# Performance work log

Hardware: AMD Instinct MI355X
Metric: run time of the kernel (lower is better)

## Reference

```python
import jax, jax.numpy as jnp
import numpy as np

TWO_PI = 2.0 * np.pi

def diff_round(x):
    # smooth differentiable rounding used throughout the repo
    return x - jnp.sin(TWO_PI * x) / TWO_PI

def harder_diff_round(x):
    return diff_round(diff_round(diff_round(x)))

def differentiable_eq(a, b):
    a = harder_diff_round(a)
    b = harder_diff_round(b)
    return harder_diff_round(a * b + (1.0 - a) * (1.0 - b))

def differentiable_and(a, b):
    return diff_round(a) * diff_round(b)

def filter_mask_of_interest(mask, initial_mask_id):
    # mask: [B, N, dx, dy, 4]; initial_mask_id: [B, N, 4]
    c = differentiable_eq(mask, initial_mask_id[:, :, None, None, :])  # [B,N,dx,dy,4]
    a = differentiable_and(c[..., 0], c[..., 1])
    b = differentiable_and(c[..., 2], c[..., 3])
    return differentiable_and(a, b)  # [B, N, dx, dy]

def get_out_image(mask_combined, initial_mask_id, resized_image):
    m = filter_mask_of_interest(mask_combined, initial_mask_id)[..., None]  # [B,N,dx,dy,1]
    masked = m * resized_image
    # per-area masked mean over (dx, dy, channel)
    num = jnp.sum(masked, axis=(2, 3, 4))           # [B, N]
    den = jnp.sum(m, axis=(2, 3, 4))                # [B, N]
    mean = num / den
    return m * mean[:, :, None, None, None]

def setup_inputs() -> dict:
    key = jax.random.key(0)
    k1, k2, k3, k4, k5 = jax.random.split(key, 5)
    B, N, DX, DY = 2, 8192, 16, 16
    return {
        "resized_image": jax.random.uniform(k1, (B, N, DX, DY, 1), jnp.float32),
        "mask_combined": jax.random.uniform(k2, (B, N, DX, DY, 4), jnp.float32),
        "mask_combined_alt": jax.random.uniform(k3, (B, N, DX, DY, 4), jnp.float32),
        "initial_mask_id": jax.random.uniform(k4, (B, N, 4), jnp.float32),
        "mask_new_bi_channel": jax.random.uniform(k5, (B, N, DX, DY, 2), jnp.float32),
        "mask_index": 0,
    }

def reference(resized_image, mask_combined, mask_combined_alt, initial_mask_id, mask_new_bi_channel, mask_index):
    # batched_v_Apply_on_single_area: nested vmap over (batch, area), vectorized here
    out_image = get_out_image(mask_combined, initial_mask_id, resized_image)
    out_image_alt = get_out_image(mask_combined_alt, initial_mask_id, resized_image)
    return (out_image, out_image_alt)
```

## Files before the change

kernel.cpp:

```cpp
#include <hip/hip_runtime.h>

#define INV_2PI 0.15915494309189535f

__device__ __forceinline__ float vsin_pinned(float x) {
    float r;
    asm volatile("v_sin_f32 %0, %1" : "=v"(r) : "v"(x));
    return r;
}

template <int N>
__device__ __forceinline__ void dround_batch(float* c) {
    float s[N];
#pragma unroll
    for (int i = 0; i < N; ++i) s[i] = vsin_pinned(c[i]);
#pragma unroll
    for (int i = 0; i < N; ++i) c[i] = __builtin_fmaf(-INV_2PI, s[i], c[i]);
}

__global__ __launch_bounds__(256) void De_conv_areas_kernel(
    const float* __restrict__ img,
    const float* __restrict__ mask,
    const float* __restrict__ mask_alt,
    const float* __restrict__ mask_id,
    float* __restrict__ out,
    float* __restrict__ out_alt,
    int n_areas)
{
    const int lane = threadIdx.x & 63;
    const int w    = blockIdx.x * (blockDim.x >> 6) + (threadIdx.x >> 6);
    const int area  = w >> 1;
    const int which = w & 1;
    if (area >= n_areas) return;

    const float* msk = which ? mask_alt : mask;
    float*       dst = which ? out_alt  : out;

    const size_t pix = (size_t)area * 256 + (size_t)lane * 4;

    float4 idv = *(const float4*)(mask_id + (size_t)area * 4);
    const float4* mp = (const float4*)(msk + pix * 4);
    float4 p0 = mp[0], p1 = mp[1], p2 = mp[2], p3 = mp[3];
    float4 im = *(const float4*)(img + pix);

    float hb[4] = { idv.x, idv.y, idv.z, idv.w };
    dround_batch<4>(hb); dround_batch<4>(hb); dround_batch<4>(hb);
    float vb[4];
#pragma unroll
    for (int k = 0; k < 4; ++k) vb[k] = 1.0f - hb[k];

    float c[16] = { p0.x, p0.y, p0.z, p0.w,  p1.x, p1.y, p1.z, p1.w,
                    p2.x, p2.y, p2.z, p2.w,  p3.x, p3.y, p3.z, p3.w };

    dround_batch<16>(c); dround_batch<16>(c); dround_batch<16>(c);

#pragma unroll
    for (int i = 0; i < 16; ++i) {
        float om = 1.0f - c[i];
        c[i] = __builtin_fmaf(c[i], hb[i & 3], om * vb[i & 3]);
    }

    dround_batch<16>(c); dround_batch<16>(c); dround_batch<16>(c);

    dround_batch<16>(c);
    float p[8];
#pragma unroll
    for (int j = 0; j < 4; ++j) {
        p[2*j]   = c[4*j]   * c[4*j+1];
        p[2*j+1] = c[4*j+2] * c[4*j+3];
    }
    dround_batch<8>(p);

    float imv[4] = { im.x, im.y, im.z, im.w };
    float m[4];
    float sm = 0.f, si = 0.f;
#pragma unroll
    for (int j = 0; j < 4; ++j) {
        m[j] = p[2*j] * p[2*j+1];
        sm += m[j]; si += m[j] * imv[j];
    }

#pragma unroll
    for (int off = 32; off; off >>= 1) {
        sm += __shfl_xor(sm, off, 64);
        si += __shfl_xor(si, off, 64);
    }

    const float mean = (sm > 0.f) ? (si / sm) : 0.f;

    float4 o;
    o.x = m[0] * mean; o.y = m[1] * mean; o.z = m[2] * mean; o.w = m[3] * mean;
    *(float4*)(dst + pix) = o;
}

extern "C" void kernel_launch(void* const* d_in, const int* in_sizes, int n_in,
                              void* d_out, int out_size, void* d_ws, size_t ws_size,
                              hipStream_t stream) {
    const float* img      = (const float*)d_in[0];
    const float* mask     = (const float*)d_in[1];
    const float* mask_alt = (const float*)d_in[2];
    const float* mask_id  = (const float*)d_in[3];

    const int n_areas = out_size / 512;
    float* out     = (float*)d_out;
    float* out_alt = out + (size_t)n_areas * 256;

    const int n_waves = n_areas * 2;
    const int waves_per_block = 4;
    const int blocks = (n_waves + waves_per_block - 1) / waves_per_block;
    De_conv_areas_kernel<<<blocks, 256, 0, stream>>>(
        img, mask, mask_alt, mask_id, out, out_alt, n_areas);
}
```

Measured before the change: 191.0 us.

## Process both mask variants per wave and share id rounding and image loads

Each wave now handles one area for both the primary and alternate masks instead of one mask per wave. The triple-rounded mask id and the image pixels are therefore computed and loaded once and reused for both outputs. The id rounding is folded into the first 20-wide sine batch, and loads and stores switch to a lane-strided pattern (float4 for masks, scalar for image and output). This halves the wave count and removes the duplicated id and image work. In exchange each thread holds more registers, which may lower occupancy, and the image reads and output writes are now scalar per lane.

```diff
diff --git a/kernel.cpp b/kernel.cpp
--- a/kernel.cpp
+++ b/kernel.cpp
@@ -17,6 +17,26 @@
     for (int i = 0; i < N; ++i) c[i] = __builtin_fmaf(-INV_2PI, s[i], c[i]);
 }
 
+__device__ __forceinline__ void filter_tail(float* c, const float* hb,
+                                            const float* vb, float* m) {
+#pragma unroll
+    for (int i = 0; i < 16; ++i) {
+        float om = 1.0f - c[i];
+        c[i] = __builtin_fmaf(c[i], hb[i & 3], om * vb[i & 3]);
+    }
+    dround_batch<16>(c); dround_batch<16>(c); dround_batch<16>(c);
+    dround_batch<16>(c);
+    float p[8];
+#pragma unroll
+    for (int j = 0; j < 4; ++j) {
+        p[2 * j]     = c[4 * j]     * c[4 * j + 1];
+        p[2 * j + 1] = c[4 * j + 2] * c[4 * j + 3];
+    }
+    dround_batch<8>(p);
+#pragma unroll
+    for (int j = 0; j < 4; ++j) m[j] = p[2 * j] * p[2 * j + 1];
+}
+
 __global__ __launch_bounds__(256) void De_conv_areas_kernel(
     const float* __restrict__ img,
     const float* __restrict__ mask,
@@ -27,69 +47,65 @@
     int n_areas)
 {
     const int lane = threadIdx.x & 63;
-    const int w    = blockIdx.x * (blockDim.x >> 6) + (threadIdx.x >> 6);
-    const int area  = w >> 1;
-    const int which = w & 1;
+    int area = blockIdx.x * (blockDim.x >> 6) + (threadIdx.x >> 6);
     if (area >= n_areas) return;
+    area = __builtin_amdgcn_readfirstlane(area);
 
-    const float* msk = which ? mask_alt : mask;
-    float*       dst = which ? out_alt  : out;
+    const size_t base = (size_t)area * 256;
 
-    const size_t pix = (size_t)area * 256 + (size_t)lane * 4;
+    const float4* mp = (const float4*)mask     + base + lane;
+    const float4* ap = (const float4*)mask_alt + base + lane;
+    const float*  ip = img + base + lane;
 
+    float4 q0 = mp[0], q1 = mp[64], q2 = mp[128], q3 = mp[192];
+    float4 a0 = ap[0], a1 = ap[64], a2 = ap[128], a3 = ap[192];
+    float  i0 = ip[0], i1 = ip[64], i2 = ip[128], i3 = ip[192];
     float4 idv = *(const float4*)(mask_id + (size_t)area * 4);
-    const float4* mp = (const float4*)(msk + pix * 4);
-    float4 p0 = mp[0], p1 = mp[1], p2 = mp[2], p3 = mp[3];
-    float4 im = *(const float4*)(img + pix);
 
-    float hb[4] = { idv.x, idv.y, idv.z, idv.w };
-    dround_batch<4>(hb); dround_batch<4>(hb); dround_batch<4>(hb);
+    float c0[20] = { idv.x, idv.y, idv.z, idv.w,
+                     q0.x, q0.y, q0.z, q0.w,  q1.x, q1.y, q1.z, q1.w,
+                     q2.x, q2.y, q2.z, q2.w,  q3.x, q3.y, q3.z, q3.w };
+    dround_batch<20>(c0); dround_batch<20>(c0); dround_batch<20>(c0);
+
+    float hb[4] = { c0[0], c0[1], c0[2], c0[3] };
     float vb[4];
 #pragma unroll
     for (int k = 0; k < 4; ++k) vb[k] = 1.0f - hb[k];
 
-    float c[16] = { p0.x, p0.y, p0.z, p0.w,  p1.x, p1.y, p1.z, p1.w,
-                    p2.x, p2.y, p2.z, p2.w,  p3.x, p3.y, p3.z, p3.w };
+    float m0[4];
+    filter_tail(c0 + 4, hb, vb, m0);
 
-    dround_batch<16>(c); dround_batch<16>(c); dround_batch<16>(c);
+    float c1[16] = { a0.x, a0.y, a0.z, a0.w,  a1.x, a1.y, a1.z, a1.w,
+                     a2.x, a2.y, a2.z, a2.w,  a3.x, a3.y, a3.z, a3.w };
+    dround_batch<16>(c1); dround_batch<16>(c1); dround_batch<16>(c1);
+    float m1[4];
+    filter_tail(c1, hb, vb, m1);
 
+    float im[4] = { i0, i1, i2, i3 };
+    float sm0 = 0.f, si0 = 0.f, sm1 = 0.f, si1 = 0.f;
 #pragma unroll
-    for (int i = 0; i < 16; ++i) {
-        float om = 1.0f - c[i];
-        c[i] = __builtin_fmaf(c[i], hb[i & 3], om * vb[i & 3]);
+    for (int j = 0; j < 4; ++j) {
+        sm0 += m0[j]; si0 += m0[j] * im[j];
+        sm1 += m1[j]; si1 += m1[j] * im[j];
+    }
+#pragma unroll
+    for (int off = 32; off; off >>= 1) {
+        sm0 += __shfl_xor(sm0, off, 64);
+        si0 += __shfl_xor(si0, off, 64);
+        sm1 += __shfl_xor(sm1, off, 64);
+        si1 += __shfl_xor(si1, off, 64);
     }
 
-    dround_batch<16>(c); dround_batch<16>(c); dround_batch<16>(c);
+    const float mean0 = (sm0 > 0.f) ? (si0 / sm0) : 0.f;
+    const float mean1 = (sm1 > 0.f) ? (si1 / sm1) : 0.f;
 
-    dround_batch<16>(c);
-    float p[8];
+    float* d0 = out     + base + lane;
+    float* d1 = out_alt + base + lane;
 #pragma unroll
-    for (int j = 0; j < 4; ++j) {
-        p[2*j]   = c[4*j]   * c[4*j+1];
-        p[2*j+1] = c[4*j+2] * c[4*j+3];
+    for (int k = 0; k < 4; ++k) {
+        d0[64 * k] = m0[k] * mean0;
+        d1[64 * k] = m1[k] * mean1;
     }
-    dround_batch<8>(p);
-
-    float imv[4] = { im.x, im.y, im.z, im.w };
-    float m[4];
-    float sm = 0.f, si = 0.f;
-#pragma unroll
-    for (int j = 0; j < 4; ++j) {
-        m[j] = p[2*j] * p[2*j+1];
-        sm += m[j]; si += m[j] * imv[j];
-    }
-
-#pragma unroll
-    for (int off = 32; off; off >>= 1) {
-        sm += __shfl_xor(sm, off, 64);
-        si += __shfl_xor(si, off, 64);
-    }
-
-    const float mean = (sm > 0.f) ? (si / sm) : 0.f;
-
-    float4 o;
-    o.x = m[0] * mean; o.y = m[1] * mean; o.z = m[2] * mean; o.w = m[3] * mean;
-    *(float4*)(dst + pix) = o;
 }
 
 extern "C" void kernel_launch(void* const* d_in, const int* in_sizes, int n_in,
@@ -104,9 +120,8 @@
     float* out     = (float*)d_out;
     float* out_alt = out + (size_t)n_areas * 256;
 
-    const int n_waves = n_areas * 2;
     const int waves_per_block = 4;
-    const int blocks = (n_waves + waves_per_block - 1) / waves_per_block;
+    const int blocks = (n_areas + waves_per_block - 1) / waves_per_block;
     De_conv_areas_kernel<<<blocks, 256, 0, stream>>>(
         img, mask, mask_alt, mask_id, out, out_alt, n_areas);
 }
```

New measurement: 196.2 us. 1.03x slower.
